# Kernel optimization log

Measured on AMD Instinct MI355X. Metric: run time of the kernel, lower is better.

Reference implementation:

```python
import jax, jax.numpy as jnp
import numpy as np
import math

D_MODEL = 512
N_TOTAL = 1024
HW = 4096
EPSILON = 0.2
NUM_HEADS = 8
D_K = D_MODEL // NUM_HEADS
BATCH = 4


def setup_inputs() -> dict:
    rng = jax.random.key(0)
    ks = jax.random.split(rng, 16)
    s = 1.0 / math.sqrt(D_MODEL)
    inp = {
        "query": jax.random.normal(ks[0], (BATCH, N_TOTAL, D_MODEL), jnp.float32),
        "key": jax.random.normal(ks[1], (BATCH, HW, D_MODEL), jnp.float32),
        "value": jax.random.normal(ks[2], (BATCH, HW, D_MODEL), jnp.float32),
        "x_tilde": jax.random.uniform(ks[3], (HW, 2), jnp.float32),
        "x_hat": jax.random.uniform(ks[4], (N_TOTAL, HW, 2), jnp.float32),
        # torch nn.Linear params: W is (out, in), y = x @ W.T + b
        "Wq": jax.random.uniform(ks[5], (D_MODEL, D_MODEL), jnp.float32, -s, s),
        "bq": jax.random.uniform(ks[6], (D_MODEL,), jnp.float32, -s, s),
        "Wk": jax.random.uniform(ks[7], (D_MODEL, D_MODEL), jnp.float32, -s, s),
        "bk": jax.random.uniform(ks[8], (D_MODEL,), jnp.float32, -s, s),
        "Wv": jax.random.uniform(ks[9], (D_MODEL, D_MODEL), jnp.float32, -s, s),
        "bv": jax.random.uniform(ks[10], (D_MODEL,), jnp.float32, -s, s),
        "Wo": jax.random.uniform(ks[11], (D_MODEL, D_MODEL), jnp.float32, -s, s),
        "bo": jax.random.uniform(ks[12], (D_MODEL,), jnp.float32, -s, s),
    }
    return inp


def _geo_mask(x_tilde, x_hat):
    # x_tilde: (HW, 2), x_hat: (N_total, HW, 2)
    diff = x_tilde[None, :, :] - x_hat            # (N, HW, 2)
    dist = jnp.sqrt(jnp.sum(diff * diff, axis=-1))  # (N, HW)
    return jnp.where(dist < EPSILON, 0.0, -jnp.inf).astype(x_hat.dtype)


def reference(query, key, value, x_tilde, x_hat, Wq, bq, Wk, bk, Wv, bv, Wo, bo):
    B = query.shape[0]
    M_geo = _geo_mask(x_tilde, x_hat)  # (N, HW)

    def heads(x, W, b):
        y = x @ W.T + b                                   # (B, L, D)
        return y.reshape(B, -1, NUM_HEADS, D_K).transpose(0, 2, 1, 3)  # (B, H, L, dk)

    Q = heads(query, Wq, bq)   # (B, H, N, dk)
    K = heads(key, Wk, bk)     # (B, H, HW, dk)
    V = heads(value, Wv, bv)   # (B, H, HW, dk)

    scores = jnp.einsum("bhnd,bhmd->bhnm", Q, K) / math.sqrt(D_K)
    scores = scores + M_geo[None, None, :, :]
    attn = jax.nn.softmax(scores, axis=-1)                # (B, H, N, HW)
    ctx = jnp.einsum("bhnm,bhmd->bhnd", attn, V)          # (B, H, N, dk)
    ctx = ctx.transpose(0, 2, 1, 3).reshape(B, -1, D_MODEL)
    out = ctx @ Wo.T + bo                                 # (B, N, D)
    return out, attn
```

## Files before the change

kernel.cpp:

```cpp
#include <hip/hip_runtime.h>
#include <cstdint>
#include <cstddef>

typedef __attribute__((ext_vector_type(4))) float f32x4;
typedef __attribute__((ext_vector_type(8))) short s16x8;
typedef __attribute__((ext_vector_type(4))) short s16x4;
typedef unsigned short u16;
typedef unsigned long long u64;

static __device__ inline u16 f2bf(float f) {
    unsigned u = __builtin_bit_cast(unsigned, f);
    u += 0x7fffu + ((u >> 16) & 1u);
    return (u16)(u >> 16);
}

static __device__ inline f32x4 mfma16(s16x8 a, s16x8 b, f32x4 c) {
    return __builtin_amdgcn_mfma_f32_16x16x32_bf16(a, b, c, 0, 0, 0);
}

static __device__ inline float redmax16(float v) {
    v = fmaxf(v, __shfl_xor(v, 1));
    v = fmaxf(v, __shfl_xor(v, 2));
    v = fmaxf(v, __shfl_xor(v, 4));
    v = fmaxf(v, __shfl_xor(v, 8));
    return v;
}
static __device__ inline float redsum16(float v) {
    v += __shfl_xor(v, 1);
    v += __shfl_xor(v, 2);
    v += __shfl_xor(v, 4);
    v += __shfl_xor(v, 8);
    return v;
}

__global__ __launch_bounds__(256) void cvt_bf16_kernel(const float* __restrict__ src,
                                                       u16* __restrict__ dst) {
    int i = (blockIdx.x * 256 + threadIdx.x) * 4;
    f32x4 v = *(const f32x4*)(src + i);
    s16x4 o;
    o[0] = (short)f2bf(v[0]); o[1] = (short)f2bf(v[1]);
    o[2] = (short)f2bf(v[2]); o[3] = (short)f2bf(v[3]);
    *(s16x4*)(dst + i) = o;
}

__global__ __launch_bounds__(256) void mask_kernel(const float* __restrict__ xt,
                                                   const float* __restrict__ xh,
                                                   u64* __restrict__ mb) {
    int tid  = threadIdx.x;
    int lane = tid & 63;
    int wv   = blockIdx.x * 4 + (tid >> 6);
    int n    = wv >> 6;
    int mbk  = wv & 63;
    int m    = (mbk << 6) + lane;
    size_t hidx = ((size_t)n * 4096 + m) * 2;
    float dx = xt[2 * m]     - xh[hidx];
    float dy = xt[2 * m + 1] - xh[hidx + 1];
    bool p = sqrtf(dx * dx + dy * dy) < 0.2f;
    u64 bal = __ballot(p);
    if (lane == 0) mb[wv] = bal;
}

template <int INF32, int MODE>
__global__ __launch_bounds__(256) void proj_kernel(const void* __restrict__ Xv,
                                                   const u16* __restrict__ Wb,
                                                   const float* __restrict__ bias,
                                                   void* __restrict__ Yv) {
    __shared__ u16 aT[64 * 72];
    __shared__ u16 bT[64 * 72];

    int tid  = threadIdx.x;
    int lane = tid & 63, w = tid >> 6, q = lane >> 4, m15 = lane & 15;
    int m0 = blockIdx.x * 64, n0 = blockIdx.y * 64;
    int rT = tid >> 2, cT = tid & 3;

    f32x4 cacc[4];
#pragma unroll
    for (int i = 0; i < 4; ++i) { f32x4 z = {0.f, 0.f, 0.f, 0.f}; cacc[i] = z; }

    for (int kb = 0; kb < 512; kb += 64) {
        if (INF32) {
            const float* X = (const float*)Xv;
#pragma unroll
            for (int j = 0; j < 4; ++j) {
                int k = cT * 4 + j * 16;
                f32x4 v = *(const f32x4*)(X + (size_t)(m0 + rT) * 512 + kb + k);
                s16x4 o;
                o[0] = (short)f2bf(v[0]); o[1] = (short)f2bf(v[1]);
                o[2] = (short)f2bf(v[2]); o[3] = (short)f2bf(v[3]);
                *(s16x4*)(aT + rT * 72 + k) = o;
            }
        } else {
            const u16* X = (const u16*)Xv;
#pragma unroll
            for (int j = 0; j < 2; ++j) {
                int k = cT * 8 + j * 32;
                s16x8 v = *(const s16x8*)(X + (size_t)(m0 + rT) * 512 + kb + k);
                *(s16x8*)(aT + rT * 72 + k) = v;
            }
        }
#pragma unroll
        for (int j = 0; j < 2; ++j) {
            int k = cT * 8 + j * 32;
            s16x8 v = *(const s16x8*)(Wb + (size_t)(n0 + rT) * 512 + kb + k);
            *(s16x8*)(bT + rT * 72 + k) = v;
        }
        __syncthreads();
#pragma unroll
        for (int kk = 0; kk < 2; ++kk) {
            s16x8 af = *(const s16x8*)(aT + (w * 16 + m15) * 72 + kk * 32 + q * 8);
#pragma unroll
            for (int nt = 0; nt < 4; ++nt) {
                s16x8 bf = *(const s16x8*)(bT + (nt * 16 + m15) * 72 + kk * 32 + q * 8);
                cacc[nt] = mfma16(af, bf, cacc[nt]);
            }
        }
        __syncthreads();
    }

#pragma unroll
    for (int nt = 0; nt < 4; ++nt) {
        int col = n0 + nt * 16 + m15;
        float bv = bias[col];
        int mbase = m0 + w * 16 + q * 4;
        if (MODE == 0) {
            u16* Y = (u16*)Yv;
#pragma unroll
            for (int r = 0; r < 4; ++r)
                Y[(size_t)(mbase + r) * 512 + col] = f2bf(cacc[nt][r] + bv);
        } else if (MODE == 2) {
            float* Y = (float*)Yv;
#pragma unroll
            for (int r = 0; r < 4; ++r)
                Y[(size_t)(mbase + r) * 512 + col] = cacc[nt][r] + bv;
        } else {
            u16* Yt = (u16*)Yv;
            int bidx = mbase >> 12, hw0 = mbase & 4095;
            int hh = col >> 6, d = col & 63;
            s16x4 o;
#pragma unroll
            for (int r = 0; r < 4; ++r) o[r] = (short)f2bf(cacc[nt][r] + bv);
            *(s16x4*)(Yt + ((size_t)((bidx << 3) + hh) * 64 + d) * 4096 + hw0) = o;
        }
    }
}

__global__ __launch_bounds__(512) void attn_kernel(const u16* __restrict__ Qb,
                                                   const u16* __restrict__ Kb,
                                                   const u16* __restrict__ Vtb,
                                                   const u64* __restrict__ mbits,
                                                   float* __restrict__ attnO,
                                                   u16* __restrict__ ctxO) {
    __shared__ u64   smask[1024];
    __shared__ float sred[8][16];
    __shared__ float srowm[16];
    __shared__ float srowi[16];
    __shared__ u16   sps[8][640];
    __shared__ float sctx[1024];

    int tid  = threadIdx.x;
    int lane = tid & 63, w = tid >> 6, q = lane >> 4, m15 = lane & 15;
    int bh = blockIdx.y, b = bh >> 3, h = bh & 7;
    int n0 = blockIdx.x * 16;

    for (int i = tid; i < 1024; i += 512) {
        smask[i] = mbits[(size_t)n0 * 64 + i];
        sctx[i]  = 0.f;
    }
    __syncthreads();

    const u16* Qp = Qb + ((size_t)(b * 1024 + n0 + m15)) * 512 + h * 64 + q * 8;
    s16x8 aQ0 = *(const s16x8*)(Qp);
    s16x8 aQ1 = *(const s16x8*)(Qp + 32);

    const u16* Kp = Kb + ((size_t)(b * 4096 + w * 512 + m15)) * 512 + h * 64 + q * 8;
    f32x4 acc[32];
#pragma unroll
    for (int t = 0; t < 32; ++t) {
        const u16* kp = Kp + (size_t)t * (16 * 512);
        s16x8 b0 = *(const s16x8*)(kp);
        s16x8 b1 = *(const s16x8*)(kp + 32);
        f32x4 c = {0.f, 0.f, 0.f, 0.f};
        c = mfma16(aQ0, b0, c);
        c = mfma16(aQ1, b1, c);
        acc[t] = c;
    }

    const float NEGINF = -__builtin_huge_valf();
    float mr[4] = {NEGINF, NEGINF, NEGINF, NEGINF};
#pragma unroll
    for (int t = 0; t < 32; ++t) {
        int c = (w << 9) + (t << 4) + m15;
        int widx = c >> 6, bit = c & 63;
#pragma unroll
        for (int r = 0; r < 4; ++r) {
            u64 mk = smask[(q * 4 + r) * 64 + widx];
            float s = acc[t][r] * 0.125f;
            s = ((mk >> bit) & 1ull) ? s : NEGINF;
            acc[t][r] = s;
            mr[r] = fmaxf(mr[r], s);
        }
    }
#pragma unroll
    for (int r = 0; r < 4; ++r) mr[r] = redmax16(mr[r]);
    if (m15 == 0) {
#pragma unroll
        for (int r = 0; r < 4; ++r) sred[w][q * 4 + r] = mr[r];
    }
    __syncthreads();
    if (tid < 16) {
        float mm = sred[0][tid];
#pragma unroll
        for (int ww = 1; ww < 8; ++ww) mm = fmaxf(mm, sred[ww][tid]);
        srowm[tid] = mm;
    }
    __syncthreads();
    float rm[4];
#pragma unroll
    for (int r = 0; r < 4; ++r) rm[r] = srowm[q * 4 + r];

    float ls[4] = {0.f, 0.f, 0.f, 0.f};
#pragma unroll
    for (int t = 0; t < 32; ++t) {
#pragma unroll
        for (int r = 0; r < 4; ++r) {
            float p = exp2f((acc[t][r] - rm[r]) * 1.4426950408889634f);
            acc[t][r] = p;
            ls[r] += p;
        }
    }
#pragma unroll
    for (int r = 0; r < 4; ++r) ls[r] = redsum16(ls[r]);
    if (m15 == 0) {
#pragma unroll
        for (int r = 0; r < 4; ++r) sred[w][q * 4 + r] = ls[r];
    }
    __syncthreads();
    if (tid < 16) {
        float ss = 0.f;
#pragma unroll
        for (int ww = 0; ww < 8; ++ww) ss += sred[ww][tid];
        srowi[tid] = 1.0f / ss;
    }
    __syncthreads();
    float iv[4];
#pragma unroll
    for (int r = 0; r < 4; ++r) iv[r] = srowi[q * 4 + r];

    float* aB[4];
#pragma unroll
    for (int r = 0; r < 4; ++r)
        aB[r] = attnO + ((size_t)(bh * 1024 + n0 + q * 4 + r)) * 4096 + (w << 9) + m15;

    const u16* Vp = Vtb + ((size_t)(bh * 64 + m15)) * 4096 + (w << 9) + q * 8;
    u16* psw = &sps[w][0];
    const u16* psr = psw + m15 * 40 + q * 8;

    f32x4 ctxa[4];
#pragma unroll
    for (int i = 0; i < 4; ++i) { f32x4 z = {0.f, 0.f, 0.f, 0.f}; ctxa[i] = z; }

#pragma unroll
    for (int cc = 0; cc < 16; ++cc) {
#pragma unroll
        for (int sub = 0; sub < 2; ++sub) {
            int t = cc * 2 + sub;
#pragma unroll
            for (int r = 0; r < 4; ++r) {
                float a = acc[t][r] * iv[r];
                aB[r][cc * 32 + sub * 16] = a;
                psw[(q * 4 + r) * 40 + sub * 16 + m15] = f2bf(a);
            }
        }
        s16x8 aP = *(const s16x8*)(psr);
#pragma unroll
        for (int dt = 0; dt < 4; ++dt) {
            s16x8 bV = *(const s16x8*)(Vp + dt * (16 * 4096) + cc * 32);
            ctxa[dt] = mfma16(aP, bV, ctxa[dt]);
        }
    }

#pragma unroll
    for (int dt = 0; dt < 4; ++dt)
#pragma unroll
        for (int r = 0; r < 4; ++r)
            atomicAdd(&sctx[(q * 4 + r) * 64 + dt * 16 + m15], ctxa[dt][r]);
    __syncthreads();
    for (int i = tid; i < 1024; i += 512) {
        int rr = i >> 6, d = i & 63;
        ctxO[((size_t)(b * 1024 + n0 + rr)) * 512 + h * 64 + d] = f2bf(sctx[i]);
    }
}

extern "C" void kernel_launch(void* const* d_in, const int* in_sizes, int n_in,
                              void* d_out, int out_size, void* d_ws, size_t ws_size,
                              hipStream_t stream) {
    (void)in_sizes; (void)n_in; (void)out_size; (void)ws_size;
    const float* query = (const float*)d_in[0];
    const float* key   = (const float*)d_in[1];
    const float* value = (const float*)d_in[2];
    const float* x_tilde = (const float*)d_in[3];
    const float* x_hat   = (const float*)d_in[4];
    const float* Wq = (const float*)d_in[5];  const float* bq = (const float*)d_in[6];
    const float* Wk = (const float*)d_in[7];  const float* bk = (const float*)d_in[8];
    const float* Wv = (const float*)d_in[9];  const float* bv = (const float*)d_in[10];
    const float* Wo = (const float*)d_in[11]; const float* bo = (const float*)d_in[12];

    char* ws = (char*)d_ws;
    u16* wq   = (u16*)(ws + 0);
    u16* wk   = (u16*)(ws + 524288);
    u16* wv   = (u16*)(ws + 1048576);
    u16* wo   = (u16*)(ws + 1572864);
    u16* Qb   = (u16*)(ws + 2097152);
    u16* Kb   = (u16*)(ws + 6291456);
    u16* Vtb  = (u16*)(ws + 23068672);
    u16* ctxb = (u16*)(ws + 39845888);
    u64* mbits = (u64*)(ws + 44040192);

    cvt_bf16_kernel<<<256, 256, 0, stream>>>(Wq, wq);
    cvt_bf16_kernel<<<256, 256, 0, stream>>>(Wk, wk);
    cvt_bf16_kernel<<<256, 256, 0, stream>>>(Wv, wv);
    cvt_bf16_kernel<<<256, 256, 0, stream>>>(Wo, wo);
    mask_kernel<<<16384, 256, 0, stream>>>(x_tilde, x_hat, mbits);

    proj_kernel<1, 0><<<dim3(64, 8),  256, 0, stream>>>(query, wq, bq, Qb);
    proj_kernel<1, 0><<<dim3(256, 8), 256, 0, stream>>>(key,   wk, bk, Kb);
    proj_kernel<1, 1><<<dim3(256, 8), 256, 0, stream>>>(value, wv, bv, Vtb);

    float* attnO = (float*)d_out + 2097152;
    attn_kernel<<<dim3(64, 32), 512, 0, stream>>>(Qb, Kb, Vtb, mbits, attnO, ctxb);

    proj_kernel<0, 2><<<dim3(64, 8), 256, 0, stream>>>(ctxb, wo, bo, d_out);
}
```

Before: 1.087 ms.

## Use head-major Q/K layouts, fold softmax scale into Wq, defer normalization and attn stores

Q and K projections now write head-major layouts so attention loads contiguous 64-element rows per head instead of strided 512-wide rows. The 1/sqrt(dk) scale is folded into the Wq conversion and the bias, and exp uses a single FMA. The mask is read directly from global memory, four words at a time, instead of being staged in shared memory, which also drops one block barrier. Unnormalized probabilities feed a double-buffered P buffer for the PV MFMA, with normalization applied to ctx at the end. The attention-probability output is written afterwards with nontemporal stores. Blocks are remapped on a 1D grid so neighbouring blocks share a query tile across heads, and the longer live range of acc may raise register pressure.

```diff
diff --git a/kernel.cpp b/kernel.cpp
--- a/kernel.cpp
+++ b/kernel.cpp
@@ -34,12 +34,12 @@
 }
 
 __global__ __launch_bounds__(256) void cvt_bf16_kernel(const float* __restrict__ src,
-                                                       u16* __restrict__ dst) {
+                                                       u16* __restrict__ dst, float scale) {
     int i = (blockIdx.x * 256 + threadIdx.x) * 4;
     f32x4 v = *(const f32x4*)(src + i);
     s16x4 o;
-    o[0] = (short)f2bf(v[0]); o[1] = (short)f2bf(v[1]);
-    o[2] = (short)f2bf(v[2]); o[3] = (short)f2bf(v[3]);
+    o[0] = (short)f2bf(v[0] * scale); o[1] = (short)f2bf(v[1] * scale);
+    o[2] = (short)f2bf(v[2] * scale); o[3] = (short)f2bf(v[3] * scale);
     *(s16x4*)(dst + i) = o;
 }
 
@@ -60,10 +60,11 @@
     if (lane == 0) mb[wv] = bal;
 }
 
-template <int INF32, int MODE>
+template <int INF32, int MODE, int LSHIFT>
 __global__ __launch_bounds__(256) void proj_kernel(const void* __restrict__ Xv,
                                                    const u16* __restrict__ Wb,
                                                    const float* __restrict__ bias,
+                                                   float bscale,
                                                    void* __restrict__ Yv) {
     __shared__ u16 aT[64 * 72];
     __shared__ u16 bT[64 * 72];
@@ -120,18 +121,23 @@
 #pragma unroll
     for (int nt = 0; nt < 4; ++nt) {
         int col = n0 + nt * 16 + m15;
-        float bv = bias[col];
+        float bv = bias[col] * bscale;
         int mbase = m0 + w * 16 + q * 4;
-        if (MODE == 0) {
-            u16* Y = (u16*)Yv;
-#pragma unroll
-            for (int r = 0; r < 4; ++r)
-                Y[(size_t)(mbase + r) * 512 + col] = f2bf(cacc[nt][r] + bv);
-        } else if (MODE == 2) {
+        if (MODE == 2) {
             float* Y = (float*)Yv;
 #pragma unroll
             for (int r = 0; r < 4; ++r)
                 Y[(size_t)(mbase + r) * 512 + col] = cacc[nt][r] + bv;
+        } else if (MODE == 3) {
+            u16* Y = (u16*)Yv;
+            int hh = col >> 6, d = col & 63;
+#pragma unroll
+            for (int r = 0; r < 4; ++r) {
+                int mg = mbase + r;
+                int bb = mg >> LSHIFT;
+                int nn = mg & ((1 << LSHIFT) - 1);
+                Y[(((size_t)(bb * 8 + hh) << LSHIFT) + nn) * 64 + d] = f2bf(cacc[nt][r] + bv);
+            }
         } else {
             u16* Yt = (u16*)Yv;
             int bidx = mbase >> 12, hw0 = mbase & 4095;
@@ -144,39 +150,36 @@
     }
 }
 
-__global__ __launch_bounds__(512) void attn_kernel(const u16* __restrict__ Qb,
-                                                   const u16* __restrict__ Kb,
-                                                   const u16* __restrict__ Vtb,
+__global__ __launch_bounds__(512) void attn_kernel(const u16* __restrict__ Qh,
+                                                   const u16* __restrict__ Kh,
+                                                   const u16* __restrict__ Vt,
                                                    const u64* __restrict__ mbits,
                                                    float* __restrict__ attnO,
                                                    u16* __restrict__ ctxO) {
-    __shared__ u64   smask[1024];
     __shared__ float sred[8][16];
     __shared__ float srowm[16];
     __shared__ float srowi[16];
-    __shared__ u16   sps[8][640];
+    __shared__ u16   sps[8][2][640];
     __shared__ float sctx[1024];
 
     int tid  = threadIdx.x;
     int lane = tid & 63, w = tid >> 6, q = lane >> 4, m15 = lane & 15;
-    int bh = blockIdx.y, b = bh >> 3, h = bh & 7;
-    int n0 = blockIdx.x * 16;
-
-    for (int i = tid; i < 1024; i += 512) {
-        smask[i] = mbits[(size_t)n0 * 64 + i];
-        sctx[i]  = 0.f;
-    }
-    __syncthreads();
-
-    const u16* Qp = Qb + ((size_t)(b * 1024 + n0 + m15)) * 512 + h * 64 + q * 8;
+    int i = blockIdx.x;
+    int bh = (i & 7) + ((i >> 3) & 3) * 8;
+    int n0 = (i >> 5) * 16;
+    int b = bh >> 3, h = bh & 7;
+
+    for (int j = tid; j < 1024; j += 512) sctx[j] = 0.f;
+
+    const u16* Qp = Qh + (((size_t)bh << 10) + n0 + m15) * 64 + q * 8;
     s16x8 aQ0 = *(const s16x8*)(Qp);
     s16x8 aQ1 = *(const s16x8*)(Qp + 32);
 
-    const u16* Kp = Kb + ((size_t)(b * 4096 + w * 512 + m15)) * 512 + h * 64 + q * 8;
+    const u16* Kp = Kh + (((size_t)bh << 12) + (w << 9) + m15) * 64 + q * 8;
     f32x4 acc[32];
 #pragma unroll
     for (int t = 0; t < 32; ++t) {
-        const u16* kp = Kp + (size_t)t * (16 * 512);
+        const u16* kp = Kp + (size_t)t * (16 * 64);
         s16x8 b0 = *(const s16x8*)(kp);
         s16x8 b1 = *(const s16x8*)(kp + 32);
         f32x4 c = {0.f, 0.f, 0.f, 0.f};
@@ -187,17 +190,24 @@
 
     const float NEGINF = -__builtin_huge_valf();
     float mr[4] = {NEGINF, NEGINF, NEGINF, NEGINF};
-#pragma unroll
-    for (int t = 0; t < 32; ++t) {
-        int c = (w << 9) + (t << 4) + m15;
-        int widx = c >> 6, bit = c & 63;
-#pragma unroll
-        for (int r = 0; r < 4; ++r) {
-            u64 mk = smask[(q * 4 + r) * 64 + widx];
-            float s = acc[t][r] * 0.125f;
-            s = ((mk >> bit) & 1ull) ? s : NEGINF;
-            acc[t][r] = s;
-            mr[r] = fmaxf(mr[r], s);
+    const u64* mrow = mbits + (size_t)n0 * 64;
+#pragma unroll
+    for (int t4 = 0; t4 < 8; ++t4) {
+        int widx = (w << 3) + t4;
+        u64 mk[4];
+#pragma unroll
+        for (int r = 0; r < 4; ++r) mk[r] = mrow[(q * 4 + r) * 64 + widx];
+#pragma unroll
+        for (int tt = 0; tt < 4; ++tt) {
+            int t = t4 * 4 + tt;
+            int bit = tt * 16 + m15;
+#pragma unroll
+            for (int r = 0; r < 4; ++r) {
+                float s = acc[t][r];
+                s = ((mk[r] >> bit) & 1ull) ? s : NEGINF;
+                acc[t][r] = s;
+                mr[r] = fmaxf(mr[r], s);
+            }
         }
     }
 #pragma unroll
@@ -214,16 +224,17 @@
         srowm[tid] = mm;
     }
     __syncthreads();
-    float rm[4];
-#pragma unroll
-    for (int r = 0; r < 4; ++r) rm[r] = srowm[q * 4 + r];
+    const float L2E = 1.44269504f;
+    float bb[4];
+#pragma unroll
+    for (int r = 0; r < 4; ++r) bb[r] = srowm[q * 4 + r] * L2E;
 
     float ls[4] = {0.f, 0.f, 0.f, 0.f};
 #pragma unroll
     for (int t = 0; t < 32; ++t) {
 #pragma unroll
         for (int r = 0; r < 4; ++r) {
-            float p = exp2f((acc[t][r] - rm[r]) * 1.4426950408889634f);
+            float p = exp2f(__builtin_fmaf(acc[t][r], L2E, -bb[r]));
             acc[t][r] = p;
             ls[r] += p;
         }
@@ -246,32 +257,25 @@
 #pragma unroll
     for (int r = 0; r < 4; ++r) iv[r] = srowi[q * 4 + r];
 
-    float* aB[4];
-#pragma unroll
-    for (int r = 0; r < 4; ++r)
-        aB[r] = attnO + ((size_t)(bh * 1024 + n0 + q * 4 + r)) * 4096 + (w << 9) + m15;
-
-    const u16* Vp = Vtb + ((size_t)(bh * 64 + m15)) * 4096 + (w << 9) + q * 8;
-    u16* psw = &sps[w][0];
-    const u16* psr = psw + m15 * 40 + q * 8;
+    const u16* Vp = Vt + (((size_t)bh << 6) + m15) * 4096 + (w << 9) + q * 8;
+    const u16* psr0 = &sps[w][0][m15 * 40 + q * 8];
+    const u16* psr1 = &sps[w][1][m15 * 40 + q * 8];
 
     f32x4 ctxa[4];
 #pragma unroll
-    for (int i = 0; i < 4; ++i) { f32x4 z = {0.f, 0.f, 0.f, 0.f}; ctxa[i] = z; }
+    for (int j = 0; j < 4; ++j) { f32x4 z = {0.f, 0.f, 0.f, 0.f}; ctxa[j] = z; }
 
 #pragma unroll
     for (int cc = 0; cc < 16; ++cc) {
+        u16* pw = &sps[w][cc & 1][0];
 #pragma unroll
         for (int sub = 0; sub < 2; ++sub) {
             int t = cc * 2 + sub;
 #pragma unroll
-            for (int r = 0; r < 4; ++r) {
-                float a = acc[t][r] * iv[r];
-                aB[r][cc * 32 + sub * 16] = a;
-                psw[(q * 4 + r) * 40 + sub * 16 + m15] = f2bf(a);
-            }
-        }
-        s16x8 aP = *(const s16x8*)(psr);
+            for (int r = 0; r < 4; ++r)
+                pw[(q * 4 + r) * 40 + sub * 16 + m15] = f2bf(acc[t][r]);
+        }
+        s16x8 aP = *(const s16x8*)((cc & 1) ? psr1 : psr0);
 #pragma unroll
         for (int dt = 0; dt < 4; ++dt) {
             s16x8 bV = *(const s16x8*)(Vp + dt * (16 * 4096) + cc * 32);
@@ -279,15 +283,23 @@
         }
     }
 
+    float* aB = attnO + (((size_t)bh << 10) + n0 + q * 4) * 4096 + (w << 9) + m15;
+#pragma unroll
+    for (int t = 0; t < 32; ++t) {
+#pragma unroll
+        for (int r = 0; r < 4; ++r)
+            __builtin_nontemporal_store(acc[t][r] * iv[r], aB + (size_t)r * 4096 + t * 16);
+    }
+
 #pragma unroll
     for (int dt = 0; dt < 4; ++dt)
 #pragma unroll
         for (int r = 0; r < 4; ++r)
-            atomicAdd(&sctx[(q * 4 + r) * 64 + dt * 16 + m15], ctxa[dt][r]);
-    __syncthreads();
-    for (int i = tid; i < 1024; i += 512) {
-        int rr = i >> 6, d = i & 63;
-        ctxO[((size_t)(b * 1024 + n0 + rr)) * 512 + h * 64 + d] = f2bf(sctx[i]);
+            atomicAdd(&sctx[(q * 4 + r) * 64 + dt * 16 + m15], ctxa[dt][r] * iv[r]);
+    __syncthreads();
+    for (int j = tid; j < 1024; j += 512) {
+        int rr = j >> 6, d = j & 63;
+        ctxO[(((size_t)b << 10) + n0 + rr) * 512 + h * 64 + d] = f2bf(sctx[j]);
     }
 }
 
@@ -310,24 +322,24 @@
     u16* wk   = (u16*)(ws + 524288);
     u16* wv   = (u16*)(ws + 1048576);
     u16* wo   = (u16*)(ws + 1572864);
-    u16* Qb   = (u16*)(ws + 2097152);
-    u16* Kb   = (u16*)(ws + 6291456);
+    u16* Qh   = (u16*)(ws + 2097152);
+    u16* Kh   = (u16*)(ws + 6291456);
     u16* Vtb  = (u16*)(ws + 23068672);
     u16* ctxb = (u16*)(ws + 39845888);
     u64* mbits = (u64*)(ws + 44040192);
 
-    cvt_bf16_kernel<<<256, 256, 0, stream>>>(Wq, wq);
-    cvt_bf16_kernel<<<256, 256, 0, stream>>>(Wk, wk);
-    cvt_bf16_kernel<<<256, 256, 0, stream>>>(Wv, wv);
-    cvt_bf16_kernel<<<256, 256, 0, stream>>>(Wo, wo);
+    cvt_bf16_kernel<<<256, 256, 0, stream>>>(Wq, wq, 0.125f);
+    cvt_bf16_kernel<<<256, 256, 0, stream>>>(Wk, wk, 1.0f);
+    cvt_bf16_kernel<<<256, 256, 0, stream>>>(Wv, wv, 1.0f);
+    cvt_bf16_kernel<<<256, 256, 0, stream>>>(Wo, wo, 1.0f);
     mask_kernel<<<16384, 256, 0, stream>>>(x_tilde, x_hat, mbits);
 
-    proj_kernel<1, 0><<<dim3(64, 8),  256, 0, stream>>>(query, wq, bq, Qb);
-    proj_kernel<1, 0><<<dim3(256, 8), 256, 0, stream>>>(key,   wk, bk, Kb);
-    proj_kernel<1, 1><<<dim3(256, 8), 256, 0, stream>>>(value, wv, bv, Vtb);
+    proj_kernel<1, 3, 10><<<dim3(64, 8),  256, 0, stream>>>(query, wq, bq, 0.125f, Qh);
+    proj_kernel<1, 3, 12><<<dim3(256, 8), 256, 0, stream>>>(key,   wk, bk, 1.0f,   Kh);
+    proj_kernel<1, 1, 12><<<dim3(256, 8), 256, 0, stream>>>(value, wv, bv, 1.0f,   Vtb);
 
     float* attnO = (float*)d_out + 2097152;
-    attn_kernel<<<dim3(64, 32), 512, 0, stream>>>(Qb, Kb, Vtb, mbits, attnO, ctxb);
-
-    proj_kernel<0, 2><<<dim3(64, 8), 256, 0, stream>>>(ctxb, wo, bo, d_out);
-}
+    attn_kernel<<<2048, 512, 0, stream>>>(Qh, Kh, Vtb, mbits, attnO, ctxb);
+
+    proj_kernel<0, 2, 10><<<dim3(64, 8), 256, 0, stream>>>(ctxb, wo, bo, 1.0f, d_out);
+}
```

Result: faster. 998.8 us (-8.2%).
